# Performance work log

Hardware: AMD Instinct MI355X
Metric: run time of the kernel (lower is better)

## Reference

```python
import jax, jax.numpy as jnp
import numpy as np
from jax import lax

SPARSITY_WEIGHT = 0.7
BETA_A = 1.0
BETA_I = 1.0
B, N, ZI, ZA = 32, 1024, 64, 128
EPS = 1e-10


def setup_inputs() -> dict:
    key = jax.random.key(0)
    ks = jax.random.split(key, 11)
    A_hat_batch = jax.random.uniform(ks[0], (B, N, N), jnp.float32, 1e-6, 1.0 - 1e-6)
    A_true = jax.random.bernoulli(ks[1], 0.05, (B, N, N)).astype(jnp.float32)
    X_hat = jnp.zeros((1,), jnp.float32)
    X_true = jnp.zeros((1,), jnp.float32)
    mu_A = jax.random.normal(ks[2], (B, ZA), jnp.float32)
    logvar_A = 0.5 * jax.random.normal(ks[3], (B, ZA), jnp.float32)
    mu_i = jax.random.normal(ks[4], (B, N, ZI), jnp.float32)
    logvar_i = 0.5 * jax.random.normal(ks[5], (B, N, ZI), jnp.float32)
    z_a = jax.random.normal(ks[6], (B, ZA), jnp.float32)
    all_B_mus = jax.random.normal(ks[7], (N, ZI, ZA), jnp.float32) * 0.1
    all_B_logvars = jax.random.normal(ks[8], (N, ZI, ZA), jnp.float32) * 0.1
    return dict(A_hat_batch=A_hat_batch, A_true=A_true, X_hat=X_hat, X_true=X_true,
                mu_A=mu_A, logvar_A=logvar_A, mu_i=mu_i, logvar_i=logvar_i,
                z_a=z_a, all_B_mus=all_B_mus, all_B_logvars=all_B_logvars)


def kl_between_two_gaussians(m1, lv1, m2, lv2):
    # Faithful to original (note: 0.5 multiplies only det ratio, and -d not -0.5*log-det form)
    det_term = jnp.exp(lv1.sum(-1) - lv2.sum(-1))  # det1/det2
    d_term = m1.shape[-1]
    trace_term = jnp.exp(lv1 - lv2).sum(-1)
    inner_prod_term = (jnp.square(m2 - m1) / jnp.exp(lv2)).sum(-1)
    return 0.5 * det_term - d_term + trace_term + inner_prod_term


def adj_recon_term(A_hat, A_true):
    A = jnp.where(A_hat == 0.0, EPS, jnp.where(A_hat == 1.0, 1.0 - EPS, A_hat))
    ll = A_true * jnp.log(A) + (1.0 - A_true) * jnp.log(1.0 - A)
    ll = jnp.where(A_true == 0.0, ll * SPARSITY_WEIGHT, ll)
    return ll.sum((-1, -2)).mean()


def reference(A_hat_batch, A_true, X_hat, X_true, mu_A, logvar_A, mu_i, logvar_i, z_a, all_B_mus, all_B_logvars):
    A_recon = adj_recon_term(A_hat_batch, A_true)
    X_recon = 0.0
    # KL_A: to standard normal prior
    zeros = jnp.zeros_like(mu_A)
    KL_A = kl_between_two_gaussians(mu_A, logvar_A, zeros, zeros).mean()
    # KL_i: vectorized over node axis (original looped per node)
    z_a_d = lax.stop_gradient(z_a)
    prior_means = lax.stop_gradient(jnp.einsum('nfg,bg->bnf', all_B_mus, z_a_d))
    prior_logvars = lax.stop_gradient(jnp.einsum('nfg,bg->bnf', all_B_logvars, z_a_d))
    node_kls = kl_between_two_gaussians(mu_i, logvar_i, prior_means, prior_logvars)  # [B, N]
    KL_i = node_kls.sum(-1).mean()
    neg_beta_elbo = -(A_recon + X_recon + BETA_A * KL_A + BETA_I * KL_i)
    return (A_recon, KL_A, KL_i, neg_beta_elbo)
```

## Files before the change

kernel.cpp:

```cpp
#include <hip/hip_runtime.h>


static constexpr int BB  = 32;
static constexpr int NN  = 1024;
static constexpr int ZIc = 64;
static constexpr int ZAc = 128;
static constexpr int AB  = 4096;
static constexpr int KB  = 1024;

#define EPSV 1e-10f
#define SPW  0.7f

__device__ __forceinline__ float ll_elem(float a, float t) {
    a = (a == 0.0f) ? EPSV : ((a == 1.0f) ? (1.0f - EPSV) : a);
    float x = (t == 0.0f) ? (1.0f - a) : a;
    float s = (t == 0.0f) ? SPW : 1.0f;
    return s * __logf(x);
}

__device__ __forceinline__ float ll4(float4 a, float4 t) {
    return ll_elem(a.x, t.x) + ll_elem(a.y, t.y) +
           ll_elem(a.z, t.z) + ll_elem(a.w, t.w);
}

__global__ __launch_bounds__(256) void arecon_kernel(
        const float4* __restrict__ Ah, const float4* __restrict__ At,
        double* __restrict__ slots) {
    const size_t base = (size_t)blockIdx.x * 2048 + threadIdx.x;

    float4 a0 = Ah[base +    0];  float4 t0 = At[base +    0];
    float4 a1 = Ah[base +  256];  float4 t1 = At[base +  256];
    float4 a2 = Ah[base +  512];  float4 t2 = At[base +  512];
    float4 a3 = Ah[base +  768];  float4 t3 = At[base +  768];
    float4 a4 = Ah[base + 1024];  float4 t4 = At[base + 1024];
    float4 a5 = Ah[base + 1280];  float4 t5 = At[base + 1280];
    float4 a6 = Ah[base + 1536];  float4 t6 = At[base + 1536];
    float4 a7 = Ah[base + 1792];  float4 t7 = At[base + 1792];
    __builtin_amdgcn_sched_barrier(0);

    float lsum = 0.0f;
    lsum += ll4(a0, t0);
    lsum += ll4(a1, t1);
    lsum += ll4(a2, t2);
    lsum += ll4(a3, t3);
    lsum += ll4(a4, t4);
    lsum += ll4(a5, t5);
    lsum += ll4(a6, t6);
    lsum += ll4(a7, t7);

#pragma unroll
    for (int m = 1; m < 64; m <<= 1) lsum += __shfl_xor(lsum, m, 64);
    __shared__ float wsum[4];
    const int lane = threadIdx.x & 63, wv = threadIdx.x >> 6;
    if (lane == 0) wsum[wv] = lsum;
    __syncthreads();
    if (threadIdx.x == 0)
        slots[blockIdx.x] = (double)(wsum[0] + wsum[1] + wsum[2] + wsum[3]);
}

__global__ __launch_bounds__(256) void kli_kernel(
        const float* __restrict__ mu_i, const float* __restrict__ lv_i,
        const float* __restrict__ z_a,
        const float* __restrict__ Bmu, const float* __restrict__ Blv,
        double* __restrict__ slots) {
    const int n    = blockIdx.x;
    const int wave = __builtin_amdgcn_readfirstlane(threadIdx.x >> 6);
    const int f    = threadIdx.x & 63;

    const float4* bmu = reinterpret_cast<const float4*>(Bmu + ((size_t)n * ZIc + f) * ZAc);
    const float4* blv = reinterpret_cast<const float4*>(Blv + ((size_t)n * ZIc + f) * ZAc);

    float pm[8], pl[8];
#pragma unroll
    for (int i = 0; i < 8; ++i) { pm[i] = 0.0f; pl[i] = 0.0f; }

    float4 mA[4], lA[4], mB[4], lB[4];
#pragma unroll
    for (int q = 0; q < 4; ++q) { mA[q] = bmu[q]; lA[q] = blv[q]; }

#define KLI_COMPUTE(MV, LV, CC)                                               \
    {                                                                         \
        _Pragma("unroll")                                                     \
        for (int bi = 0; bi < 8; ++bi) {                                      \
            const int b = wave * 8 + bi;                                      \
            const float* zp = z_a + b * ZAc + (CC) * 16;                      \
            _Pragma("unroll")                                                 \
            for (int q = 0; q < 4; ++q) {                                     \
                float4 zz = *reinterpret_cast<const float4*>(zp + 4 * q);     \
                pm[bi] += MV[q].x * zz.x + MV[q].y * zz.y +                   \
                          MV[q].z * zz.z + MV[q].w * zz.w;                    \
                pl[bi] += LV[q].x * zz.x + LV[q].y * zz.y +                   \
                          LV[q].z * zz.z + LV[q].w * zz.w;                    \
            }                                                                 \
        }                                                                     \
    }

#pragma unroll 1
    for (int c = 0; c < 8; c += 2) {
#pragma unroll
        for (int q = 0; q < 4; ++q) { mB[q] = bmu[(c + 1) * 4 + q]; lB[q] = blv[(c + 1) * 4 + q]; }
        KLI_COMPUTE(mA, lA, c)
        if (c + 2 < 8) {
#pragma unroll
            for (int q = 0; q < 4; ++q) { mA[q] = bmu[(c + 2) * 4 + q]; lA[q] = blv[(c + 2) * 4 + q]; }
        }
        KLI_COMPUTE(mB, lB, c + 1)
    }
#undef KLI_COMPUTE

    double local = 0.0;
#pragma unroll
    for (int bi = 0; bi < 8; ++bi) {
        const int b = wave * 8 + bi;
        const size_t base = ((size_t)b * NN + n) * ZIc + f;
        float m1  = mu_i[base];
        float lv1 = lv_i[base];
        float d   = lv1 - pl[bi];
        float dm  = pm[bi] - m1;
        float sc  = __expf(d) + dm * dm * __expf(-pl[bi]);
        float sd  = d;
#pragma unroll
        for (int m = 1; m < 64; m <<= 1) {
            sd += __shfl_xor(sd, m, 64);
            sc += __shfl_xor(sc, m, 64);
        }
        if (f == 0)
            local += (double)(0.5f * __expf(sd) - 64.0f + sc);
    }
    __shared__ double wacc[4];
    if (f == 0) wacc[wave] = local;
    __syncthreads();
    if (threadIdx.x == 0)
        slots[n] = wacc[0] + wacc[1] + wacc[2] + wacc[3];
}

__global__ __launch_bounds__(256) void finalize_kernel(
        const double* __restrict__ ws,
        const float* __restrict__ mu_A, const float* __restrict__ lv_A,
        float* __restrict__ out) {
    const int lane = threadIdx.x & 63;
    const int wave = threadIdx.x >> 6;

    double a = 0.0, ki = 0.0;
    const double2* w2 = reinterpret_cast<const double2*>(ws);
    for (int i = threadIdx.x; i < AB / 2; i += 256) { double2 v = w2[i]; a += v.x + v.y; }
    for (int i = threadIdx.x; i < KB / 2; i += 256) { double2 v = w2[AB / 2 + i]; ki += v.x + v.y; }
#pragma unroll
    for (int m = 1; m < 64; m <<= 1) {
        a  += __shfl_xor(a, m, 64);
        ki += __shfl_xor(ki, m, 64);
    }

    double ka = 0.0;
#pragma unroll 1
    for (int bb = 0; bb < 8; ++bb) {
        const int b = wave * 8 + bb;
        float lv0 = lv_A[b * ZAc + lane], lv1 = lv_A[b * ZAc + 64 + lane];
        float m0  = mu_A[b * ZAc + lane], m1  = mu_A[b * ZAc + 64 + lane];
        float slv = lv0 + lv1;
        float sc  = __expf(lv0) + __expf(lv1) + m0 * m0 + m1 * m1;
#pragma unroll
        for (int m = 1; m < 64; m <<= 1) {
            slv += __shfl_xor(slv, m, 64);
            sc  += __shfl_xor(sc, m, 64);
        }
        if (lane == 0)
            ka += (double)(0.5f * __expf(slv) - 128.0f + sc);
    }

    __shared__ double sa[4], ski[4], ska[4];
    if (lane == 0) { sa[wave] = a; ski[wave] = ki; ska[wave] = ka; }
    __syncthreads();
    if (threadIdx.x == 0) {
        double A  = (sa[0] + sa[1] + sa[2] + sa[3]) / 32.0;
        double KI = (ski[0] + ski[1] + ski[2] + ski[3]) / 32.0;
        double KA = (ska[0] + ska[1] + ska[2] + ska[3]) / 32.0;
        out[0] = (float)A;
        out[1] = (float)KA;
        out[2] = (float)KI;
        out[3] = (float)(-(A + KA + KI));
    }
}

extern "C" void kernel_launch(void* const* d_in, const int* in_sizes, int n_in,
                              void* d_out, int out_size, void* d_ws, size_t ws_size,
                              hipStream_t stream) {
    const float* Ah   = (const float*)d_in[0];
    const float* At   = (const float*)d_in[1];
    const float* mu_A = (const float*)d_in[4];
    const float* lv_A = (const float*)d_in[5];
    const float* mu_i = (const float*)d_in[6];
    const float* lv_i = (const float*)d_in[7];
    const float* z_a  = (const float*)d_in[8];
    const float* Bmu  = (const float*)d_in[9];
    const float* Blv  = (const float*)d_in[10];

    double* ws = (double*)d_ws;
    float* out = (float*)d_out;

    hipLaunchKernelGGL(arecon_kernel, dim3(AB), dim3(256), 0, stream,
                       (const float4*)Ah, (const float4*)At, ws);
    hipLaunchKernelGGL(kli_kernel, dim3(KB), dim3(256), 0, stream,
                       mu_i, lv_i, z_a, Bmu, Blv, ws + AB);
    hipLaunchKernelGGL(finalize_kernel, dim3(1), dim3(256), 0, stream,
                       ws, mu_A, lv_A, out);
}
```

Measured before the change: 368.5 us.

## Stage A-recon inputs into LDS with double-buffered async global_load_lds

Rewrites the adjacency reconstruction kernel so it no longer loads sixteen float4 values per thread directly into registers. It now uses async global-to-LDS copies into a double buffer, loops over eight rounds and prefetches the next round while computing the current one. Each block now covers twice as much data, so the grid is halved and the finalize kernel reads fewer partial sums. The trade-off is fewer bytes in flight per thread, a block barrier every round, and extra LDS traffic, which may hurt a kernel that is purely bandwidth-bound.

Measured after the change: 375.1 us. About the same (+1.8%).

```diff
diff --git a/kernel.cpp b/kernel.cpp
--- a/kernel.cpp
+++ b/kernel.cpp
@@ -5,7 +5,7 @@
 static constexpr int NN  = 1024;
 static constexpr int ZIc = 64;
 static constexpr int ZAc = 128;
-static constexpr int AB  = 4096;
+static constexpr int AB2 = 2048;
 static constexpr int KB  = 1024;
 
 #define EPSV 1e-10f
@@ -23,38 +23,59 @@
            ll_elem(a.z, t.z) + ll_elem(a.w, t.w);
 }
 
+__device__ __forceinline__ void stage16(const float4* g, float4* l) {
+    __builtin_amdgcn_global_load_lds(
+        (const __attribute__((address_space(1))) void*)g,
+        (__attribute__((address_space(3))) void*)l, 16, 0, 0);
+}
+
 __global__ __launch_bounds__(256) void arecon_kernel(
         const float4* __restrict__ Ah, const float4* __restrict__ At,
         double* __restrict__ slots) {
-    const size_t base = (size_t)blockIdx.x * 2048 + threadIdx.x;
-
-    float4 a0 = Ah[base +    0];  float4 t0 = At[base +    0];
-    float4 a1 = Ah[base +  256];  float4 t1 = At[base +  256];
-    float4 a2 = Ah[base +  512];  float4 t2 = At[base +  512];
-    float4 a3 = Ah[base +  768];  float4 t3 = At[base +  768];
-    float4 a4 = Ah[base + 1024];  float4 t4 = At[base + 1024];
-    float4 a5 = Ah[base + 1280];  float4 t5 = At[base + 1280];
-    float4 a6 = Ah[base + 1536];  float4 t6 = At[base + 1536];
-    float4 a7 = Ah[base + 1792];  float4 t7 = At[base + 1792];
-    __builtin_amdgcn_sched_barrier(0);
+    __shared__ float4 bufA[2][512];
+    __shared__ float4 bufT[2][512];
+    const int tid  = threadIdx.x;
+    const int lane = tid & 63;
+    const int w    = tid >> 6;
+    const size_t base4 = (size_t)blockIdx.x * 4096;
+
+    const int o0 = w * 128 + lane;
+    const int o1 = o0 + 64;
+
+#define STAGE(R, PB)                                                          \
+    {                                                                         \
+        const float4* gA = Ah + base4 + (size_t)(R) * 512;                    \
+        const float4* gT = At + base4 + (size_t)(R) * 512;                    \
+        stage16(gA + o0, &bufA[PB][o0]);                                      \
+        stage16(gA + o1, &bufA[PB][o1]);                                      \
+        stage16(gT + o0, &bufT[PB][o0]);                                      \
+        stage16(gT + o1, &bufT[PB][o1]);                                      \
+    }
+
+    STAGE(0, 0)
+    __syncthreads();
 
     float lsum = 0.0f;
-    lsum += ll4(a0, t0);
-    lsum += ll4(a1, t1);
-    lsum += ll4(a2, t2);
-    lsum += ll4(a3, t3);
-    lsum += ll4(a4, t4);
-    lsum += ll4(a5, t5);
-    lsum += ll4(a6, t6);
-    lsum += ll4(a7, t7);
+#pragma unroll 1
+    for (int r = 0; r < 8; ++r) {
+        const int cur = r & 1;
+        if (r + 1 < 8) STAGE(r + 1, cur ^ 1)
+        float4 a0 = bufA[cur][tid];
+        float4 t0 = bufT[cur][tid];
+        float4 a1 = bufA[cur][256 + tid];
+        float4 t1 = bufT[cur][256 + tid];
+        lsum += ll4(a0, t0);
+        lsum += ll4(a1, t1);
+        __syncthreads();
+    }
+#undef STAGE
 
 #pragma unroll
     for (int m = 1; m < 64; m <<= 1) lsum += __shfl_xor(lsum, m, 64);
     __shared__ float wsum[4];
-    const int lane = threadIdx.x & 63, wv = threadIdx.x >> 6;
-    if (lane == 0) wsum[wv] = lsum;
-    __syncthreads();
-    if (threadIdx.x == 0)
+    if (lane == 0) wsum[w] = lsum;
+    __syncthreads();
+    if (tid == 0)
         slots[blockIdx.x] = (double)(wsum[0] + wsum[1] + wsum[2] + wsum[3]);
 }
 
@@ -143,8 +164,8 @@
 
     double a = 0.0, ki = 0.0;
     const double2* w2 = reinterpret_cast<const double2*>(ws);
-    for (int i = threadIdx.x; i < AB / 2; i += 256) { double2 v = w2[i]; a += v.x + v.y; }
-    for (int i = threadIdx.x; i < KB / 2; i += 256) { double2 v = w2[AB / 2 + i]; ki += v.x + v.y; }
+    for (int i = threadIdx.x; i < AB2 / 2; i += 256) { double2 v = w2[i]; a += v.x + v.y; }
+    for (int i = threadIdx.x; i < KB / 2; i += 256) { double2 v = w2[AB2 / 2 + i]; ki += v.x + v.y; }
 #pragma unroll
     for (int m = 1; m < 64; m <<= 1) {
         a  += __shfl_xor(a, m, 64);
@@ -198,10 +219,10 @@
     double* ws = (double*)d_ws;
     float* out = (float*)d_out;
 
-    hipLaunchKernelGGL(arecon_kernel, dim3(AB), dim3(256), 0, stream,
+    hipLaunchKernelGGL(arecon_kernel, dim3(AB2), dim3(256), 0, stream,
                        (const float4*)Ah, (const float4*)At, ws);
     hipLaunchKernelGGL(kli_kernel, dim3(KB), dim3(256), 0, stream,
-                       mu_i, lv_i, z_a, Bmu, Blv, ws + AB);
+                       mu_i, lv_i, z_a, Bmu, Blv, ws + AB2);
     hipLaunchKernelGGL(finalize_kernel, dim3(1), dim3(256), 0, stream,
                        ws, mu_A, lv_A, out);
 }
```
